# Kernel optimization log

Hardware: AMD Instinct MI355X
Metric: run time of the kernel (lower is better)

## Reference

```python
import jax, jax.numpy as jnp
import numpy as np

N = 256
FEAT = 1024           # box_head.fc7.out_features
HID_REL = 256         # RelationProposalNetwork hidden_dim
GCN_HID = 256         # gcn_hidden
HEADS = 4
NUM_PARTS = 20
OUT = NUM_PARTS + 1
TOPK = 3
IN_GCN = FEAT + 4


def setup_inputs() -> dict:
    key = jax.random.key(0)
    ks = jax.random.split(key, 16)
    features = jax.random.normal(ks[0], (N, FEAT), jnp.float32)
    # valid pixel-space boxes (x1, y1, x2, y2) inside an 800x800 image
    xy = jax.random.uniform(ks[1], (N, 2), jnp.float32, 0.0, 700.0)
    wh = jax.random.uniform(ks[2], (N, 2), jnp.float32, 8.0, 100.0)
    boxes = jnp.concatenate([xy, xy + wh], axis=1)
    s = 0.02
    W_fc1 = jax.random.normal(ks[3], (2 * FEAT + 4, HID_REL), jnp.float32) * s
    b_fc1 = jnp.zeros((HID_REL,), jnp.float32)
    W_fc2 = jax.random.normal(ks[4], (HID_REL, 1), jnp.float32) * s
    b_fc2 = jnp.zeros((1,), jnp.float32)
    W1 = jax.random.normal(ks[5], (IN_GCN, HEADS * GCN_HID), jnp.float32) * s
    a_src1 = jax.random.normal(ks[6], (HEADS, GCN_HID), jnp.float32) * s
    a_dst1 = jax.random.normal(ks[7], (HEADS, GCN_HID), jnp.float32) * s
    b1 = jnp.zeros((HEADS * GCN_HID,), jnp.float32)
    W2 = jax.random.normal(ks[8], (HEADS * GCN_HID, OUT), jnp.float32) * s
    a_src2 = jax.random.normal(ks[9], (1, OUT), jnp.float32) * s
    a_dst2 = jax.random.normal(ks[10], (1, OUT), jnp.float32) * s
    b2 = jnp.zeros((OUT,), jnp.float32)
    return {
        "features": features, "boxes": boxes,
        "W_fc1": W_fc1, "b_fc1": b_fc1, "W_fc2": W_fc2, "b_fc2": b_fc2,
        "W1": W1, "a_src1": a_src1, "a_dst1": a_dst1, "b1": b1,
        "W2": W2, "a_src2": a_src2, "a_dst2": a_dst2, "b2": b2,
        "img_h": 800, "img_w": 800,
    }


def _gat_layer(x, W, a_src, a_dst, bias, s, t, n, heads, ch):
    # PyG GATConv: message flows edge_index[0] (s) -> edge_index[1] (t),
    # softmax over incoming edges of each target node t.
    h = (x @ W).reshape(n, heads, ch)                       # [n, H, C]
    e = jax.nn.leaky_relu(
        jnp.einsum("ehc,hc->eh", h[s], a_src)
        + jnp.einsum("ehc,hc->eh", h[t], a_dst), 0.2)        # [E, H]
    m = jnp.full((n, heads), -1e30, e.dtype).at[t].max(e)    # segment max
    p = jnp.exp(e - m[t])
    denom = jax.ops.segment_sum(p, t, num_segments=n)
    alpha = p / denom[t]                                     # [E, H]
    out = jax.ops.segment_sum(alpha[:, :, None] * h[s], t, num_segments=n)
    return out.reshape(n, heads * ch) + bias


def _forward(features, boxes, W_fc1, b_fc1, W_fc2, b_fc2,
             W1, a_src1, a_dst1, b1, W2, a_src2, a_dst2, b2, img_h, img_w):
    n = features.shape[0]
    # --- RelationProposalNetwork: dense O(N^2) pairwise MLP ---
    f1 = jnp.broadcast_to(features[:, None, :], (n, n, FEAT))
    f2 = jnp.broadcast_to(features[None, :, :], (n, n, FEAT))
    geom = jnp.abs(boxes[:, None, :] - boxes[None, :, :])    # [n, n, 4]
    pair = jnp.concatenate([f1, f2, geom], axis=-1)          # [n, n, 2052]
    hid = jax.nn.relu(pair @ W_fc1 + b_fc1)                  # [n, n, 256]
    rel = (hid @ W_fc2 + b_fc2)[..., 0]                      # [n, n]
    # --- top-k graph construction (drop first = self, as in source) ---
    idx = jax.lax.top_k(rel, TOPK + 1)[1][:, 1:]             # [n, topk]
    s_e = jnp.repeat(jnp.arange(n), TOPK)                    # edge_index[0]
    t_e = idx.reshape(-1)                                    # edge_index[1]
    loops = jnp.arange(n)                                    # GATConv add_self_loops
    s_e = jnp.concatenate([s_e, loops])
    t_e = jnp.concatenate([t_e, loops])
    # --- normalized box geometry node features ---
    scale = jnp.array([img_w, img_h, img_w, img_h], jnp.float32)
    nb = boxes / scale
    geomn = jnp.stack([nb[:, 0], nb[:, 1], nb[:, 2] - nb[:, 0], nb[:, 3] - nb[:, 1]], axis=1)
    gcn_in = jnp.concatenate([features, geomn], axis=1)      # [n, 1028]
    # --- AttentionalGCN: GAT(heads=4) -> ReLU -> GAT(heads=1) ---
    h1 = jax.nn.relu(_gat_layer(gcn_in, W1, a_src1, a_dst1, b1, s_e, t_e, n, HEADS, GCN_HID))
    logits = _gat_layer(h1, W2, a_src2, a_dst2, b2, s_e, t_e, n, 1, OUT)
    return logits


def reference(features, boxes, W_fc1, b_fc1, W_fc2, b_fc2,
              W1, a_src1, a_dst1, b1, W2, a_src2, a_dst2, b2, img_h, img_w):
    logits = _forward(features, boxes, W_fc1, b_fc1, W_fc2, b_fc2,
                      W1, a_src1, a_dst1, b1, W2, a_src2, a_dst2, b2, img_h, img_w)
    labels = jnp.argmax(logits, axis=1)
    return logits, labels
```

## Files before the change

### kernel.cpp

```cpp
#include <hip/hip_runtime.h>
#include <math.h>

#define NN 256
#define FEAT 1024
#define HIDR 256
#define GCNH 256
#define M1 1024
#define OUTC 21
#define MAXDEG (NN + 1)
#define KC 16
#define KCH (FEAT / KC)
#define RB 16
#define FCOLS 1536


__global__ __launch_bounds__(256) void k_big(
        const float* __restrict__ feat, const float* __restrict__ Wfc1,
        const float* __restrict__ W1, float* __restrict__ P) {
    int id = blockIdx.x;
    int xcd = id & 7, slot = id >> 3;
    int g = xcd + 8 * (slot >> 4);
    int rg = slot & 15;
    int cgy = g >> 4, kc = g & 15;
    __shared__ float fS[RB][KCH];
    int tid = threadIdx.x;
    int r0 = rg * RB, k0 = kc * KCH;
    for (int x = tid; x < RB * KCH; x += 256) {
        int r = x >> 6, kk = x & (KCH - 1);
        fS[r][kk] = feat[(size_t)(r0 + r) * FEAT + k0 + kk];
    }
    __syncthreads();
    int gc = cgy * 512 + tid * 2;
    const float* pW;
    int ld;
    if (gc < 256)      { pW = Wfc1 + (size_t)k0 * HIDR + gc;                  ld = HIDR; }
    else if (gc < 512) { pW = Wfc1 + (size_t)(FEAT + k0) * HIDR + (gc - 256); ld = HIDR; }
    else               { pW = W1   + (size_t)k0 * M1 + (gc - 512);            ld = M1;   }
    float2 acc[RB];
#pragma unroll
    for (int r = 0; r < RB; r++) { acc[r].x = 0.f; acc[r].y = 0.f; }
    float2 w0 = *(const float2*)(pW);
    float2 w1 = *(const float2*)(pW + ld);
    float2 w2 = *(const float2*)(pW + 2 * ld);
    float2 w3 = *(const float2*)(pW + 3 * ld);
    for (int kk = 0; kk < KCH; kk += 4) {
        pW += 4 * ld;
        float2 n0 = *(const float2*)(pW);
        float2 n1 = *(const float2*)(pW + ld);
        float2 n2 = *(const float2*)(pW + 2 * ld);
        float2 n3 = *(const float2*)(pW + 3 * ld);
#pragma unroll
        for (int r = 0; r < RB; r++) {
            float4 f = *(const float4*)&fS[r][kk];
            acc[r].x = fmaf(f.x, w0.x, acc[r].x); acc[r].y = fmaf(f.x, w0.y, acc[r].y);
            acc[r].x = fmaf(f.y, w1.x, acc[r].x); acc[r].y = fmaf(f.y, w1.y, acc[r].y);
            acc[r].x = fmaf(f.z, w2.x, acc[r].x); acc[r].y = fmaf(f.z, w2.y, acc[r].y);
            acc[r].x = fmaf(f.w, w3.x, acc[r].x); acc[r].y = fmaf(f.w, w3.y, acc[r].y);
        }
        w0 = n0; w1 = n1; w2 = n2; w3 = n3;
    }
    float* Pp = P + ((size_t)r0 * KC + kc) * FCOLS + gc;
#pragma unroll
    for (int r = 0; r < RB; r++)
        *(float2*)(Pp + (size_t)r * KC * FCOLS) = acc[r];
}

__global__ __launch_bounds__(384) void k_stA(
        const float* __restrict__ P, const float* __restrict__ bfc1,
        const float* __restrict__ boxes, const int* __restrict__ imh,
        const int* __restrict__ imw, const float* __restrict__ W1,
        const float* __restrict__ as1, const float* __restrict__ ad1,
        float* __restrict__ A, float* __restrict__ BT4,
        float* __restrict__ hpre, float* __restrict__ es1,
        float* __restrict__ ed1) {
    __shared__ float gS[4];
    int row = blockIdx.x, tid = threadIdx.x;
    int c4 = tid * 4;
    const float* p = P + (size_t)row * (KC * FCOLS) + c4;
    float4 a0 = *(const float4*)(p);
    float4 a1 = *(const float4*)(p + FCOLS);
    float4 a2 = *(const float4*)(p + 2 * FCOLS);
    float4 a3 = *(const float4*)(p + 3 * FCOLS);
#pragma unroll
    for (int q = 4; q < KC; q += 4) {
        float4 t0 = *(const float4*)(p + (size_t)q * FCOLS);
        float4 t1 = *(const float4*)(p + (size_t)(q + 1) * FCOLS);
        float4 t2 = *(const float4*)(p + (size_t)(q + 2) * FCOLS);
        float4 t3 = *(const float4*)(p + (size_t)(q + 3) * FCOLS);
        a0.x += t0.x; a0.y += t0.y; a0.z += t0.z; a0.w += t0.w;
        a1.x += t1.x; a1.y += t1.y; a1.z += t1.z; a1.w += t1.w;
        a2.x += t2.x; a2.y += t2.y; a2.z += t2.z; a2.w += t2.w;
        a3.x += t3.x; a3.y += t3.y; a3.z += t3.z; a3.w += t3.w;
    }
    float4 s4;
    s4.x = (a0.x + a1.x) + (a2.x + a3.x);
    s4.y = (a0.y + a1.y) + (a2.y + a3.y);
    s4.z = (a0.z + a1.z) + (a2.z + a3.z);
    s4.w = (a0.w + a1.w) + (a2.w + a3.w);
    if (tid == 0) {
        float w = (float)imw[0], h = (float)imh[0];
        float x1 = boxes[row * 4 + 0] / w, y1 = boxes[row * 4 + 1] / h;
        float x2 = boxes[row * 4 + 2] / w, y2 = boxes[row * 4 + 3] / h;
        gS[0] = x1; gS[1] = y1; gS[2] = x2 - x1; gS[3] = y2 - y1;
    }
    __syncthreads();
    if (c4 < 256) {
        float4 bv = *(const float4*)(bfc1 + c4);
        s4.x += bv.x; s4.y += bv.y; s4.z += bv.z; s4.w += bv.w;
        *(float4*)(A + (size_t)row * HIDR + c4) = s4;
    } else if (c4 < 512) {
        int kk = c4 - 256;
        *(float4*)(BT4 + (size_t)(kk >> 2) * (NN * 4) + row * 4) = s4;
    } else {
        int ch = c4 - 512;
        float g0 = gS[0], g1 = gS[1], g2 = gS[2], g3 = gS[3];
        float4 wv;
        wv = *(const float4*)(W1 + (size_t)(FEAT + 0) * M1 + ch);
        s4.x = fmaf(g0, wv.x, s4.x); s4.y = fmaf(g0, wv.y, s4.y);
        s4.z = fmaf(g0, wv.z, s4.z); s4.w = fmaf(g0, wv.w, s4.w);
        wv = *(const float4*)(W1 + (size_t)(FEAT + 1) * M1 + ch);
        s4.x = fmaf(g1, wv.x, s4.x); s4.y = fmaf(g1, wv.y, s4.y);
        s4.z = fmaf(g1, wv.z, s4.z); s4.w = fmaf(g1, wv.w, s4.w);
        wv = *(const float4*)(W1 + (size_t)(FEAT + 2) * M1 + ch);
        s4.x = fmaf(g2, wv.x, s4.x); s4.y = fmaf(g2, wv.y, s4.y);
        s4.z = fmaf(g2, wv.z, s4.z); s4.w = fmaf(g2, wv.w, s4.w);
        wv = *(const float4*)(W1 + (size_t)(FEAT + 3) * M1 + ch);
        s4.x = fmaf(g3, wv.x, s4.x); s4.y = fmaf(g3, wv.y, s4.y);
        s4.z = fmaf(g3, wv.z, s4.z); s4.w = fmaf(g3, wv.w, s4.w);
        *(float4*)(hpre + (size_t)row * M1 + ch) = s4;
        float4 a = *(const float4*)(as1 + ch);
        float4 bv = *(const float4*)(ad1 + ch);
        float ps = s4.x * a.x + s4.y * a.y + s4.z * a.z + s4.w * a.w;
        float pd = s4.x * bv.x + s4.y * bv.y + s4.z * bv.z + s4.w * bv.w;
#pragma unroll
        for (int o = 32; o > 0; o >>= 1) {
            ps += __shfl_down(ps, o);
            pd += __shfl_down(pd, o);
        }
        if ((tid & 63) == 0) {
            int head = (tid - 128) >> 6;
            es1[row * 4 + head] = ps;
            ed1[row * 4 + head] = pd;
        }
    }
}

__global__ __launch_bounds__(512) void k_stB(
        const float* __restrict__ A, const float* __restrict__ boxes,
        const float* __restrict__ Wfc1, const float* __restrict__ Wfc2,
        const float* __restrict__ BT4, int* __restrict__ idxTop) {
    __shared__ float As[HIDR];
    __shared__ float sval[512];
    __shared__ unsigned long long swk[8];
    __shared__ int win;
    int row = blockIdx.x, tid = threadIdx.x;
    if (tid < 256) As[tid] = A[(size_t)row * HIDR + tid];
    int j = tid & 255;
    float bi0 = boxes[row * 4 + 0], bi1 = boxes[row * 4 + 1];
    float bi2 = boxes[row * 4 + 2], bi3 = boxes[row * 4 + 3];
    float g0 = fabsf(bi0 - boxes[j * 4 + 0]);
    float g1 = fabsf(bi1 - boxes[j * 4 + 1]);
    float g2 = fabsf(bi2 - boxes[j * 4 + 2]);
    float g3 = fabsf(bi3 - boxes[j * 4 + 3]);
    __syncthreads();
    {
        int half = __builtin_amdgcn_readfirstlane(tid >> 8);
        int k0 = half * 128;
        const float* pB  = BT4 + (size_t)(k0 >> 2) * (NN * 4) + j * 4;
        const float* pA  = As + k0;
        const float* pW2 = Wfc2 + k0;
        const float* pg0 = Wfc1 + (size_t)(2 * FEAT + 0) * HIDR + k0;
        const float* pg1 = Wfc1 + (size_t)(2 * FEAT + 1) * HIDR + k0;
        const float* pg2 = Wfc1 + (size_t)(2 * FEAT + 2) * HIDR + k0;
        const float* pg3 = Wfc1 + (size_t)(2 * FEAT + 3) * HIDR + k0;
        float acc = 0.f;
#pragma unroll 4
        for (int kk = 0; kk < 128; kk += 4) {
            float4 a4 = *(const float4*)(pA + kk);
            float4 w4 = *(const float4*)(pW2 + kk);
            float4 q0 = *(const float4*)(pg0 + kk);
            float4 q1 = *(const float4*)(pg1 + kk);
            float4 q2 = *(const float4*)(pg2 + kk);
            float4 q3 = *(const float4*)(pg3 + kk);
            float4 b4 = *(const float4*)pB;
            pB += NN * 4;
            float v;
            v = a4.x + b4.x; v = fmaf(g0, q0.x, v); v = fmaf(g1, q1.x, v);
            v = fmaf(g2, q2.x, v); v = fmaf(g3, q3.x, v);
            acc = fmaf(fmaxf(v, 0.f), w4.x, acc);
            v = a4.y + b4.y; v = fmaf(g0, q0.y, v); v = fmaf(g1, q1.y, v);
            v = fmaf(g2, q2.y, v); v = fmaf(g3, q3.y, v);
            acc = fmaf(fmaxf(v, 0.f), w4.y, acc);
            v = a4.z + b4.z; v = fmaf(g0, q0.z, v); v = fmaf(g1, q1.z, v);
            v = fmaf(g2, q2.z, v); v = fmaf(g3, q3.z, v);
            acc = fmaf(fmaxf(v, 0.f), w4.z, acc);
            v = a4.w + b4.w; v = fmaf(g0, q0.w, v); v = fmaf(g1, q1.w, v);
            v = fmaf(g2, q2.w, v); v = fmaf(g3, q3.w, v);
            acc = fmaf(fmaxf(v, 0.f), w4.w, acc);
        }
        sval[tid] = acc;
    }
    __syncthreads();
    if (tid < 256) sval[tid] = sval[tid] + sval[tid + 256];
    __syncthreads();
    for (int r = 0; r < 4; r++) {
        unsigned long long key = 0ULL;
        if (tid < 256) {
            unsigned u = __float_as_uint(sval[tid]);
            u = (u & 0x80000000u) ? ~u : (u | 0x80000000u);
            key = ((unsigned long long)u << 32) | (unsigned)(NN - 1 - tid);
        }
#pragma unroll
        for (int o = 32; o > 0; o >>= 1) {
            unsigned long long nk = __shfl_down(key, o);
            if (nk > key) key = nk;
        }
        if ((tid & 63) == 0) swk[tid >> 6] = key;
        __syncthreads();
        if (tid == 0) {
            unsigned long long m = swk[0];
#pragma unroll
            for (int q = 1; q < 8; q++) if (swk[q] > m) m = swk[q];
            int wj = NN - 1 - (int)(m & 0xFFFFFFFFu);
            win = wj;
            if (r > 0) idxTop[row * 3 + (r - 1)] = wj;
        }
        __syncthreads();
        if (tid == win) sval[tid] = -1e38f;
        __syncthreads();
    }
}

__global__ __launch_bounds__(512) void k_stC(
        const int* __restrict__ idxTop, const float* __restrict__ es1,
        const float* __restrict__ ed1, const float* __restrict__ hpre,
        const float* __restrict__ b1, const float* __restrict__ W2,
        const float* __restrict__ as2, const float* __restrict__ ad2,
        int* __restrict__ deg, int* __restrict__ inlist,
        float* __restrict__ h2, float* __restrict__ es2,
        float* __restrict__ ed2) {
    __shared__ float sval[512];
    __shared__ int pfxw[4];
    __shared__ int lst[MAXDEG];
    __shared__ int dgS;
    __shared__ float sc[MAXDEG * 4];
    __shared__ float sh[M1];
    __shared__ float part[24 * OUTC];
    __shared__ float h2row[OUTC];
    int row = blockIdx.x, tid = threadIdx.x;
    int f = 0;
    if (tid < 256)
        f = (idxTop[tid * 3 + 0] == row) | (idxTop[tid * 3 + 1] == row)
          | (idxTop[tid * 3 + 2] == row);
    unsigned long long bm = __ballot(f);
    int lane = tid & 63, wv6 = tid >> 6;
    int rank = __popcll(bm & ((1ULL << lane) - 1ULL));
    if (tid < 256 && lane == 0) pfxw[wv6] = __popcll(bm);
    __syncthreads();
    {
        int base = 0;
#pragma unroll
        for (int w = 0; w < 4; w++) base += (w < wv6) ? pfxw[w] : 0;
        if (tid < 256 && f) {
            lst[base + rank] = tid;
            inlist[row * MAXDEG + base + rank] = tid;
        }
    }
    if (tid == 0) {
        int tot = pfxw[0] + pfxw[1] + pfxw[2] + pfxw[3];
        lst[tot] = row;
        inlist[row * MAXDEG + tot] = row;
        dgS = tot + 1;
        deg[row] = tot + 1;
    }
    __syncthreads();
    int dg = dgS;
    for (int p = tid; p < dg * 4; p += 512) {
        int e = p >> 2, hq2 = p & 3;
        int s = lst[e];
        float v = es1[s * 4 + hq2] + ed1[row * 4 + hq2];
        sc[p] = v >= 0.f ? v : 0.2f * v;
    }
    __syncthreads();
    int hq = tid & 3;
    {
        float lm = -1e30f;
        for (int e = tid >> 2; e < dg; e += 128)
            lm = fmaxf(lm, sc[e * 4 + hq]);
#pragma unroll
        for (int o = 4; o <= 32; o <<= 1) lm = fmaxf(lm, __shfl_xor(lm, o));
        if (lane < 4) sval[wv6 * 4 + hq] = lm;
        __syncthreads();
        float m = sval[hq];
#pragma unroll
        for (int w = 1; w < 8; w++) m = fmaxf(m, sval[w * 4 + hq]);
        float ls = 0.f;
        for (int e = tid >> 2; e < dg; e += 128) {
            float pv = expf(sc[e * 4 + hq] - m);
            sc[e * 4 + hq] = pv;
            ls += pv;
        }
#pragma unroll
        for (int o = 4; o <= 32; o <<= 1) ls += __shfl_xor(ls, o);
        if (lane < 4) sval[32 + wv6 * 4 + hq] = ls;
        __syncthreads();
        float den = sval[32 + hq];
#pragma unroll
        for (int w = 1; w < 8; w++) den += sval[32 + w * 4 + hq];
        for (int e = tid >> 2; e < dg; e += 128)
            sc[e * 4 + hq] = sc[e * 4 + hq] / den;
    }
    __syncthreads();
    {
        int col = tid & 255, hh = (tid >> 8) * 2;
        float acc0 = 0.f, acc1 = 0.f;
        int e = 0;
        for (; e + 8 <= dg; e += 8) {
            float v0[8], v1[8];
#pragma unroll
            for (int u = 0; u < 8; u++) {
                const float* hs = hpre + (size_t)lst[e + u] * M1;
                v0[u] = hs[hh * GCNH + col];
                v1[u] = hs[(hh + 1) * GCNH + col];
            }
#pragma unroll
            for (int u = 0; u < 8; u++) {
                acc0 = fmaf(sc[(e + u) * 4 + hh],     v0[u], acc0);
                acc1 = fmaf(sc[(e + u) * 4 + hh + 1], v1[u], acc1);
            }
        }
        for (; e < dg; e++) {
            const float* hs = hpre + (size_t)lst[e] * M1;
            acc0 = fmaf(sc[e * 4 + hh],     hs[hh * GCNH + col],       acc0);
            acc1 = fmaf(sc[e * 4 + hh + 1], hs[(hh + 1) * GCNH + col], acc1);
        }
        int c0 = hh * GCNH + col, c1 = (hh + 1) * GCNH + col;
        sh[c0] = fmaxf(acc0 + b1[c0], 0.f);
        sh[c1] = fmaxf(acc1 + b1[c1], 0.f);
    }
    __syncthreads();
    if (tid < 504) {
        int o = tid % OUTC, pq = tid / OUTC;
        float a2 = 0.f;
        for (int d = pq; d < M1; d += 24)
            a2 = fmaf(sh[d], W2[d * OUTC + o], a2);
        part[pq * OUTC + o] = a2;
    }
    __syncthreads();
    if (tid < OUTC) {
        float ssum = 0.f;
        for (int pq = 0; pq < 24; pq++) ssum += part[pq * OUTC + tid];
        h2[row * OUTC + tid] = ssum;
        h2row[tid] = ssum;
    }
    __syncthreads();
    if (tid == 0) {
        float ssum = 0.f, dd = 0.f;
        for (int k = 0; k < OUTC; k++) {
            ssum = fmaf(h2row[k], as2[k], ssum);
            dd = fmaf(h2row[k], ad2[k], dd);
        }
        es2[row] = ssum;
        ed2[row] = dd;
    }
}

__global__ __launch_bounds__(512) void k_stD(
        const int* __restrict__ deg, const int* __restrict__ inlist,
        const float* __restrict__ es2, const float* __restrict__ ed2,
        const float* __restrict__ h2, const float* __restrict__ b2,
        float* __restrict__ out) {
    __shared__ float sval[512];
    __shared__ int lst[MAXDEG];
    __shared__ float scD[MAXDEG];
    __shared__ float part[24 * OUTC];
    __shared__ float lv[OUTC];
    int row = blockIdx.x, tid = threadIdx.x;
    int lane = tid & 63, wv6 = tid >> 6;
    int dgT = deg[row];
    float edt = ed2[row];
    for (int p = tid; p < dgT; p += 512) {
        int s = inlist[row * MAXDEG + p];
        lst[p] = s;
        float v = es2[s] + edt;
        scD[p] = v >= 0.f ? v : 0.2f * v;
    }
    __syncthreads();
    {
        float lm = -1e30f;
        for (int p = tid; p < dgT; p += 512) lm = fmaxf(lm, scD[p]);
#pragma unroll
        for (int o = 1; o <= 32; o <<= 1) lm = fmaxf(lm, __shfl_xor(lm, o));
        if (lane == 0) sval[wv6] = lm;
        __syncthreads();
        float m = sval[0];
#pragma unroll
        for (int w = 1; w < 8; w++) m = fmaxf(m, sval[w]);
        float ls = 0.f;
        for (int p = tid; p < dgT; p += 512) {
            float pv = expf(scD[p] - m);
            scD[p] = pv;
            ls += pv;
        }
#pragma unroll
        for (int o = 1; o <= 32; o <<= 1) ls += __shfl_xor(ls, o);
        if (lane == 0) sval[8 + wv6] = ls;
        __syncthreads();
        float den = sval[8];
#pragma unroll
        for (int w = 1; w < 8; w++) den += sval[8 + w];
        __syncthreads();
        if (tid < 504) {
            int o = tid % OUTC, eg = tid / OUTC;
            float acc = 0.f;
            for (int e = eg; e < dgT; e += 24) {
                int s = lst[e];
                acc = fmaf(scD[e], h2[(size_t)s * OUTC + o], acc);
            }
            part[eg * OUTC + o] = acc;
        }
        __syncthreads();
        if (tid < OUTC) {
            float ssum = 0.f;
            for (int eg = 0; eg < 24; eg++) ssum += part[eg * OUTC + tid];
            float v = ssum / den + b2[tid];
            out[row * OUTC + tid] = v;
            lv[tid] = v;
        }
    }
    __syncthreads();
    if (tid == 0) {
        int best = 0;
        float bv = lv[0];
        for (int o = 1; o < OUTC; o++)
            if (lv[o] > bv) { bv = lv[o]; best = o; }
        out[NN * OUTC + row] = (float)best;
    }
}

extern "C" void kernel_launch(void* const* d_in, const int* in_sizes, int n_in,
                              void* d_out, int out_size, void* d_ws,
                              size_t ws_size, hipStream_t stream) {
    const float* feat  = (const float*)d_in[0];
    const float* boxes = (const float*)d_in[1];
    const float* Wfc1  = (const float*)d_in[2];
    const float* bfc1  = (const float*)d_in[3];
    const float* Wfc2  = (const float*)d_in[4];
    const float* bfc2  = (const float*)d_in[5];   (void)bfc2;
    const float* W1    = (const float*)d_in[6];
    const float* as1   = (const float*)d_in[7];
    const float* ad1   = (const float*)d_in[8];
    const float* b1    = (const float*)d_in[9];
    const float* W2    = (const float*)d_in[10];
    const float* as2   = (const float*)d_in[11];
    const float* ad2   = (const float*)d_in[12];
    const float* b2    = (const float*)d_in[13];
    const int*   imh   = (const int*)d_in[14];
    const int*   imw   = (const int*)d_in[15];

    float* ws = (float*)d_ws;
    float* P     = ws;  ws += KC * NN * FCOLS;
    float* A     = ws;  ws += NN * HIDR;
    float* BT4   = ws;  ws += NN * HIDR;
    float* hpre  = ws;  ws += NN * M1;
    float* es1   = ws;  ws += NN * 4;
    float* ed1   = ws;  ws += NN * 4;
    float* h2    = ws;  ws += NN * OUTC;
    float* es2   = ws;  ws += NN;
    float* ed2   = ws;  ws += NN;
    int* idxTop  = (int*)ws;
    int* deg     = idxTop + NN * 3;
    int* inlist  = deg + NN;

    float* out = (float*)d_out;

    k_big<<<768, 256, 0, stream>>>(feat, Wfc1, W1, P);
    k_stA<<<NN, 384, 0, stream>>>(P, bfc1, boxes, imh, imw, W1, as1, ad1,
                                  A, BT4, hpre, es1, ed1);
    k_stB<<<NN, 512, 0, stream>>>(A, boxes, Wfc1, Wfc2, BT4, idxTop);
    k_stC<<<NN, 512, 0, stream>>>(idxTop, es1, ed1, hpre, b1, W2, as2, ad2,
                                  deg, inlist, h2, es2, ed2);
    k_stD<<<NN, 512, 0, stream>>>(deg, inlist, es2, ed2, h2, b2, out);
}
```

Before: 141.7 us.

## Replace split-K GEMM with in-block K reduction and fuse epilogue into GEMM

The big feature GEMM is retiled to 8-row by 64-column blocks, with the four K quarters reduced in shared memory inside each block. This removes the 16-way split-K partial buffer and the separate stage-A reduction kernel. The bias, transposed BT4 layout and box-geometry terms are now applied in the GEMM epilogue, and the attention-score dot products move into k_stB. This saves one kernel launch and a large global round-trip of partial sums. In exchange, each thread now computes one column over 8 rows, which gives less register reuse of the weights, and the output stores are scalar.

```diff
diff --git a/kernel.cpp b/kernel.cpp
--- a/kernel.cpp
+++ b/kernel.cpp
@@ -8,153 +8,124 @@
 #define M1 1024
 #define OUTC 21
 #define MAXDEG (NN + 1)
-#define KC 16
-#define KCH (FEAT / KC)
-#define RB 16
 #define FCOLS 1536
-
-
-__global__ __launch_bounds__(256) void k_big(
+#define GBM 8
+#define GBN 64
+#define GKS 4
+
+
+__global__ __launch_bounds__(256) void k_gemm(
         const float* __restrict__ feat, const float* __restrict__ Wfc1,
-        const float* __restrict__ W1, float* __restrict__ P) {
+        const float* __restrict__ W1, const float* __restrict__ boxes,
+        const int* __restrict__ imh, const int* __restrict__ imw,
+        const float* __restrict__ bfc1, float* __restrict__ A,
+        float* __restrict__ BT4, float* __restrict__ hpre) {
+    __shared__ float fS[GBM][FEAT];
+    __shared__ float part[GKS][GBM][GBN];
+    __shared__ float gmS[GBM][4];
     int id = blockIdx.x;
     int xcd = id & 7, slot = id >> 3;
-    int g = xcd + 8 * (slot >> 4);
-    int rg = slot & 15;
-    int cgy = g >> 4, kc = g & 15;
-    __shared__ float fS[RB][KCH];
+    int cg = xcd + 8 * (slot >> 5);
+    int rg = slot & 31;
+    int r0 = rg * GBM, c0 = cg * GBN;
     int tid = threadIdx.x;
-    int r0 = rg * RB, k0 = kc * KCH;
-    for (int x = tid; x < RB * KCH; x += 256) {
-        int r = x >> 6, kk = x & (KCH - 1);
-        fS[r][kk] = feat[(size_t)(r0 + r) * FEAT + k0 + kk];
-    }
-    __syncthreads();
-    int gc = cgy * 512 + tid * 2;
+    for (int x = tid * 4; x < GBM * FEAT; x += 1024) {
+        int r = x >> 10, k = x & (FEAT - 1);
+        *(float4*)&fS[r][k] = *(const float4*)(feat + (size_t)(r0 + r) * FEAT + k);
+    }
+    __syncthreads();
+    int c = tid & 63, kq = tid >> 6;
+    int gc = c0 + c;
     const float* pW;
-    int ld;
-    if (gc < 256)      { pW = Wfc1 + (size_t)k0 * HIDR + gc;                  ld = HIDR; }
-    else if (gc < 512) { pW = Wfc1 + (size_t)(FEAT + k0) * HIDR + (gc - 256); ld = HIDR; }
-    else               { pW = W1   + (size_t)k0 * M1 + (gc - 512);            ld = M1;   }
-    float2 acc[RB];
-#pragma unroll
-    for (int r = 0; r < RB; r++) { acc[r].x = 0.f; acc[r].y = 0.f; }
-    float2 w0 = *(const float2*)(pW);
-    float2 w1 = *(const float2*)(pW + ld);
-    float2 w2 = *(const float2*)(pW + 2 * ld);
-    float2 w3 = *(const float2*)(pW + 3 * ld);
-    for (int kk = 0; kk < KCH; kk += 4) {
-        pW += 4 * ld;
-        float2 n0 = *(const float2*)(pW);
-        float2 n1 = *(const float2*)(pW + ld);
-        float2 n2 = *(const float2*)(pW + 2 * ld);
-        float2 n3 = *(const float2*)(pW + 3 * ld);
-#pragma unroll
-        for (int r = 0; r < RB; r++) {
-            float4 f = *(const float4*)&fS[r][kk];
-            acc[r].x = fmaf(f.x, w0.x, acc[r].x); acc[r].y = fmaf(f.x, w0.y, acc[r].y);
-            acc[r].x = fmaf(f.y, w1.x, acc[r].x); acc[r].y = fmaf(f.y, w1.y, acc[r].y);
-            acc[r].x = fmaf(f.z, w2.x, acc[r].x); acc[r].y = fmaf(f.z, w2.y, acc[r].y);
-            acc[r].x = fmaf(f.w, w3.x, acc[r].x); acc[r].y = fmaf(f.w, w3.y, acc[r].y);
-        }
-        w0 = n0; w1 = n1; w2 = n2; w3 = n3;
-    }
-    float* Pp = P + ((size_t)r0 * KC + kc) * FCOLS + gc;
-#pragma unroll
-    for (int r = 0; r < RB; r++)
-        *(float2*)(Pp + (size_t)r * KC * FCOLS) = acc[r];
+    int ldW;
+    if (gc < 256)      { pW = Wfc1 + gc;                            ldW = HIDR; }
+    else if (gc < 512) { pW = Wfc1 + (size_t)FEAT * HIDR + (gc - 256); ldW = HIDR; }
+    else               { pW = W1 + (gc - 512);                      ldW = M1; }
+    const float* pk = pW + (size_t)(kq * 256) * ldW;
+    float acc[GBM];
+#pragma unroll
+    for (int r = 0; r < GBM; r++) acc[r] = 0.f;
+    int kbeg = kq * 256;
+    for (int k = kbeg; k < kbeg + 256; k += 8) {
+        float w[8];
+#pragma unroll
+        for (int u = 0; u < 8; u++) w[u] = pk[(size_t)u * ldW];
+        pk += 8 * (size_t)ldW;
+#pragma unroll
+        for (int r = 0; r < GBM; r++) {
+            float4 f = *(const float4*)&fS[r][k];
+            float4 h = *(const float4*)&fS[r][k + 4];
+            float a = acc[r];
+            a = fmaf(f.x, w[0], a); a = fmaf(f.y, w[1], a);
+            a = fmaf(f.z, w[2], a); a = fmaf(f.w, w[3], a);
+            a = fmaf(h.x, w[4], a); a = fmaf(h.y, w[5], a);
+            a = fmaf(h.z, w[6], a); a = fmaf(h.w, w[7], a);
+            acc[r] = a;
+        }
+    }
+#pragma unroll
+    for (int r = 0; r < GBM; r++) part[kq][r][c] = acc[r];
+    if (c0 >= 512 && tid < GBM) {
+        float w = (float)imw[0], h = (float)imh[0];
+        float x1 = boxes[(r0 + tid) * 4 + 0] / w;
+        float y1 = boxes[(r0 + tid) * 4 + 1] / h;
+        float x2 = boxes[(r0 + tid) * 4 + 2] / w;
+        float y2 = boxes[(r0 + tid) * 4 + 3] / h;
+        gmS[tid][0] = x1; gmS[tid][1] = y1;
+        gmS[tid][2] = x2 - x1; gmS[tid][3] = y2 - y1;
+    }
+    __syncthreads();
+    for (int o = tid; o < GBM * GBN; o += 256) {
+        int r = o >> 6, cc = o & 63;
+        float v = (part[0][r][cc] + part[1][r][cc])
+                + (part[2][r][cc] + part[3][r][cc]);
+        int gc2 = c0 + cc, grow = r0 + r;
+        if (c0 < 256) {
+            v += bfc1[gc2];
+            A[(size_t)grow * HIDR + gc2] = v;
+        } else if (c0 < 512) {
+            int kk = gc2 - 256;
+            BT4[(size_t)(kk >> 2) * (NN * 4) + grow * 4 + (kk & 3)] = v;
+        } else {
+            int ch = gc2 - 512;
+            v = fmaf(gmS[r][0], W1[(size_t)(FEAT + 0) * M1 + ch], v);
+            v = fmaf(gmS[r][1], W1[(size_t)(FEAT + 1) * M1 + ch], v);
+            v = fmaf(gmS[r][2], W1[(size_t)(FEAT + 2) * M1 + ch], v);
+            v = fmaf(gmS[r][3], W1[(size_t)(FEAT + 3) * M1 + ch], v);
+            hpre[(size_t)grow * M1 + ch] = v;
+        }
+    }
 }
 
-__global__ __launch_bounds__(384) void k_stA(
-        const float* __restrict__ P, const float* __restrict__ bfc1,
-        const float* __restrict__ boxes, const int* __restrict__ imh,
-        const int* __restrict__ imw, const float* __restrict__ W1,
+__global__ __launch_bounds__(512) void k_stB(
+        const float* __restrict__ A, const float* __restrict__ boxes,
+        const float* __restrict__ Wfc1, const float* __restrict__ Wfc2,
+        const float* __restrict__ BT4, const float* __restrict__ hpre,
         const float* __restrict__ as1, const float* __restrict__ ad1,
-        float* __restrict__ A, float* __restrict__ BT4,
-        float* __restrict__ hpre, float* __restrict__ es1,
+        int* __restrict__ idxTop, float* __restrict__ es1,
         float* __restrict__ ed1) {
-    __shared__ float gS[4];
+    __shared__ float As[HIDR];
+    __shared__ float sval[512];
+    __shared__ unsigned long long swk[8];
+    __shared__ float swE[8], swD[8];
+    __shared__ int win;
     int row = blockIdx.x, tid = threadIdx.x;
-    int c4 = tid * 4;
-    const float* p = P + (size_t)row * (KC * FCOLS) + c4;
-    float4 a0 = *(const float4*)(p);
-    float4 a1 = *(const float4*)(p + FCOLS);
-    float4 a2 = *(const float4*)(p + 2 * FCOLS);
-    float4 a3 = *(const float4*)(p + 3 * FCOLS);
-#pragma unroll
-    for (int q = 4; q < KC; q += 4) {
-        float4 t0 = *(const float4*)(p + (size_t)q * FCOLS);
-        float4 t1 = *(const float4*)(p + (size_t)(q + 1) * FCOLS);
-        float4 t2 = *(const float4*)(p + (size_t)(q + 2) * FCOLS);
-        float4 t3 = *(const float4*)(p + (size_t)(q + 3) * FCOLS);
-        a0.x += t0.x; a0.y += t0.y; a0.z += t0.z; a0.w += t0.w;
-        a1.x += t1.x; a1.y += t1.y; a1.z += t1.z; a1.w += t1.w;
-        a2.x += t2.x; a2.y += t2.y; a2.z += t2.z; a2.w += t2.w;
-        a3.x += t3.x; a3.y += t3.y; a3.z += t3.z; a3.w += t3.w;
-    }
-    float4 s4;
-    s4.x = (a0.x + a1.x) + (a2.x + a3.x);
-    s4.y = (a0.y + a1.y) + (a2.y + a3.y);
-    s4.z = (a0.z + a1.z) + (a2.z + a3.z);
-    s4.w = (a0.w + a1.w) + (a2.w + a3.w);
-    if (tid == 0) {
-        float w = (float)imw[0], h = (float)imh[0];
-        float x1 = boxes[row * 4 + 0] / w, y1 = boxes[row * 4 + 1] / h;
-        float x2 = boxes[row * 4 + 2] / w, y2 = boxes[row * 4 + 3] / h;
-        gS[0] = x1; gS[1] = y1; gS[2] = x2 - x1; gS[3] = y2 - y1;
-    }
-    __syncthreads();
-    if (c4 < 256) {
-        float4 bv = *(const float4*)(bfc1 + c4);
-        s4.x += bv.x; s4.y += bv.y; s4.z += bv.z; s4.w += bv.w;
-        *(float4*)(A + (size_t)row * HIDR + c4) = s4;
-    } else if (c4 < 512) {
-        int kk = c4 - 256;
-        *(float4*)(BT4 + (size_t)(kk >> 2) * (NN * 4) + row * 4) = s4;
-    } else {
-        int ch = c4 - 512;
-        float g0 = gS[0], g1 = gS[1], g2 = gS[2], g3 = gS[3];
-        float4 wv;
-        wv = *(const float4*)(W1 + (size_t)(FEAT + 0) * M1 + ch);
-        s4.x = fmaf(g0, wv.x, s4.x); s4.y = fmaf(g0, wv.y, s4.y);
-        s4.z = fmaf(g0, wv.z, s4.z); s4.w = fmaf(g0, wv.w, s4.w);
-        wv = *(const float4*)(W1 + (size_t)(FEAT + 1) * M1 + ch);
-        s4.x = fmaf(g1, wv.x, s4.x); s4.y = fmaf(g1, wv.y, s4.y);
-        s4.z = fmaf(g1, wv.z, s4.z); s4.w = fmaf(g1, wv.w, s4.w);
-        wv = *(const float4*)(W1 + (size_t)(FEAT + 2) * M1 + ch);
-        s4.x = fmaf(g2, wv.x, s4.x); s4.y = fmaf(g2, wv.y, s4.y);
-        s4.z = fmaf(g2, wv.z, s4.z); s4.w = fmaf(g2, wv.w, s4.w);
-        wv = *(const float4*)(W1 + (size_t)(FEAT + 3) * M1 + ch);
-        s4.x = fmaf(g3, wv.x, s4.x); s4.y = fmaf(g3, wv.y, s4.y);
-        s4.z = fmaf(g3, wv.z, s4.z); s4.w = fmaf(g3, wv.w, s4.w);
-        *(float4*)(hpre + (size_t)row * M1 + ch) = s4;
-        float4 a = *(const float4*)(as1 + ch);
-        float4 bv = *(const float4*)(ad1 + ch);
-        float ps = s4.x * a.x + s4.y * a.y + s4.z * a.z + s4.w * a.w;
-        float pd = s4.x * bv.x + s4.y * bv.y + s4.z * bv.z + s4.w * bv.w;
+    if (tid < 256) As[tid] = A[(size_t)row * HIDR + tid];
+    {
+        const float* hp = hpre + (size_t)row * M1;
+        int ch = tid * 2;
+        float2 hv = *(const float2*)(hp + ch);
+        float2 av = *(const float2*)(as1 + ch);
+        float2 dv = *(const float2*)(ad1 + ch);
+        float ps = hv.x * av.x + hv.y * av.y;
+        float pd = hv.x * dv.x + hv.y * dv.y;
 #pragma unroll
         for (int o = 32; o > 0; o >>= 1) {
             ps += __shfl_down(ps, o);
             pd += __shfl_down(pd, o);
         }
-        if ((tid & 63) == 0) {
-            int head = (tid - 128) >> 6;
-            es1[row * 4 + head] = ps;
-            ed1[row * 4 + head] = pd;
-        }
-    }
-}
-
-__global__ __launch_bounds__(512) void k_stB(
-        const float* __restrict__ A, const float* __restrict__ boxes,
-        const float* __restrict__ Wfc1, const float* __restrict__ Wfc2,
-        const float* __restrict__ BT4, int* __restrict__ idxTop) {
-    __shared__ float As[HIDR];
-    __shared__ float sval[512];
-    __shared__ unsigned long long swk[8];
-    __shared__ int win;
-    int row = blockIdx.x, tid = threadIdx.x;
-    if (tid < 256) As[tid] = A[(size_t)row * HIDR + tid];
+        if ((tid & 63) == 0) { swE[tid >> 6] = ps; swD[tid >> 6] = pd; }
+    }
     int j = tid & 255;
     float bi0 = boxes[row * 4 + 0], bi1 = boxes[row * 4 + 1];
     float bi2 = boxes[row * 4 + 2], bi3 = boxes[row * 4 + 3];
@@ -163,6 +134,10 @@
     float g2 = fabsf(bi2 - boxes[j * 4 + 2]);
     float g3 = fabsf(bi3 - boxes[j * 4 + 3]);
     __syncthreads();
+    if (tid < 4) {
+        es1[row * 4 + tid] = swE[2 * tid] + swE[2 * tid + 1];
+        ed1[row * 4 + tid] = swD[2 * tid] + swD[2 * tid + 1];
+    }
     {
         int half = __builtin_amdgcn_readfirstlane(tid >> 8);
         int k0 = half * 128;
@@ -459,7 +434,6 @@
     const int*   imw   = (const int*)d_in[15];
 
     float* ws = (float*)d_ws;
-    float* P     = ws;  ws += KC * NN * FCOLS;
     float* A     = ws;  ws += NN * HIDR;
     float* BT4   = ws;  ws += NN * HIDR;
     float* hpre  = ws;  ws += NN * M1;
@@ -474,10 +448,10 @@
 
     float* out = (float*)d_out;
 
-    k_big<<<768, 256, 0, stream>>>(feat, Wfc1, W1, P);
-    k_stA<<<NN, 384, 0, stream>>>(P, bfc1, boxes, imh, imw, W1, as1, ad1,
-                                  A, BT4, hpre, es1, ed1);
-    k_stB<<<NN, 512, 0, stream>>>(A, boxes, Wfc1, Wfc2, BT4, idxTop);
+    k_gemm<<<(NN / GBM) * (FCOLS / GBN), 256, 0, stream>>>(
+        feat, Wfc1, W1, boxes, imh, imw, bfc1, A, BT4, hpre);
+    k_stB<<<NN, 512, 0, stream>>>(A, boxes, Wfc1, Wfc2, BT4, hpre,
+                                  as1, ad1, idxTop, es1, ed1);
     k_stC<<<NN, 512, 0, stream>>>(idxTop, es1, ed1, hpre, b1, W2, as2, ad2,
                                   deg, inlist, h2, es2, ed2);
     k_stD<<<NN, 512, 0, stream>>>(deg, inlist, es2, ed2, h2, b2, out);
```

After: 140.5 us. About the same (-0.9%).
